# Kernel optimization log

Measured on AMD Instinct MI355X. Metric: run time of the kernel, lower is better.

The kernel has to match this reference:

```python
import jax, jax.numpy as jnp
import numpy as np

BATCH = 16
D_MODEL = 384
STATE = 64          # state_dim
D_INNER = 384       # ssd_expand * d_model
H = 64
W = 64


def setup_inputs() -> dict:
    key = jax.random.key(0)
    ks = jax.random.split(key, 6)
    x = jax.random.normal(ks[0], (BATCH, D_MODEL, H * W), jnp.float32)
    # 1x1 Conv1d weights stored as 2D matrices [out_ch, in_ch]
    W_bcdt = jax.random.normal(ks[1], (3 * STATE, D_MODEL), jnp.float32) / np.sqrt(D_MODEL).astype(np.float32)
    # depthwise 3x3 conv, groups = 3*STATE -> kernel [3S, 1, 3, 3]
    W_dw = jax.random.normal(ks[2], (3 * STATE, 1, 3, 3), jnp.float32) / 3.0
    W_hz = jax.random.normal(ks[3], (2 * D_INNER, D_MODEL), jnp.float32) / np.sqrt(D_MODEL).astype(np.float32)
    W_out = jax.random.normal(ks[4], (D_MODEL, D_INNER), jnp.float32) / np.sqrt(D_INNER).astype(np.float32)
    A_param = jax.random.uniform(ks[5], (STATE,), jnp.float32, 1.0, 16.0)
    D_param = jnp.ones((1,), jnp.float32)
    return {"x": x, "W_bcdt": W_bcdt, "W_dw": W_dw, "W_hz": W_hz,
            "W_out": W_out, "A_param": A_param, "D_param": D_param,
            "size_h": H, "size_w": W}


def reference(x, W_bcdt, W_dw, W_hz, W_out, A_param, D_param, size_h, size_w):
    b, d, L = x.shape
    S = A_param.shape[0]
    # BCdt_proj: 1x1 conv1d == matmul over channel dim -> [b, 3S, L]
    bcdt = jnp.einsum('od,bdl->bol', W_bcdt, x)
    # depthwise 3x3 conv over the spatial view [b, 3S, H, W]
    xhw = bcdt.reshape(b, 3 * S, size_h, size_w)
    xhw = jax.lax.conv_general_dilated(
        xhw, W_dw, window_strides=(1, 1), padding='SAME',
        dimension_numbers=('NCHW', 'OIHW', 'NCHW'),
        feature_group_count=3 * S)
    bcdt = xhw.reshape(b, 3 * S, L)
    Bm, Cm, dt = jnp.split(bcdt, 3, axis=1)          # each [b, S, L]
    # softmax over the sequence dim with learned A offset
    A = jax.nn.softmax(dt + A_param[None, :, None], axis=-1)
    AB = A * Bm                                       # [b, S, L]
    h = jnp.einsum('bdl,bsl->bds', x, AB)             # x @ AB^T -> [b, d, S]
    hz = jnp.einsum('od,bds->bos', W_hz, h)           # hz_proj -> [b, 2*d_inner, S]
    h1, z = jnp.split(hz, 2, axis=1)                  # each [b, d_inner, S]
    hgate = h1 * jax.nn.silu(z) + h1 * D_param[0]
    hout = jnp.einsum('oe,bes->bos', W_out, hgate)    # out_proj -> [b, d, S]
    y = jnp.einsum('bds,bsl->bdl', hout, Cm)          # h @ C -> [b, d, L]
    y = y.reshape(b, d, size_h, size_w)
    return (y, hout)
```

## Files before the change

kernel.cpp:

```cpp
#include <hip/hip_runtime.h>

typedef unsigned short u16;
typedef short s16x8 __attribute__((ext_vector_type(8)));
typedef float f32x4 __attribute__((ext_vector_type(4)));

#define NB 16
#define DMODEL 384
#define SDIM 64
#define LSEQ 4096
#define C3S 192

__device__ __forceinline__ float b2f(u16 u) {
    union { unsigned int i; float f; } v; v.i = ((unsigned int)u) << 16; return v.f;
}
__device__ __forceinline__ u16 f2b(float f) {
    union { float ff; unsigned int i; } v; v.ff = f;
    unsigned int x = v.i;
    unsigned int r = (x + 0x7fffu + ((x >> 16) & 1u)) >> 16;
    return (u16)r;
}

__global__ __launch_bounds__(256) void kcvt(const float* __restrict__ x,
                                            u16* __restrict__ xbT) {
    __shared__ __align__(16) u16 T[64][72];
    const int t = threadIdx.x;
    const int l0 = blockIdx.x * 64;
    const int d0 = blockIdx.y * 64;
    const int b = blockIdx.z;
    const int dr = t >> 2;
    const int lo = (t & 3) * 16;
    const float* xp = x + ((size_t)(b * DMODEL + d0 + dr)) * LSEQ + l0 + lo;
    float4 x0 = *reinterpret_cast<const float4*>(xp + 0);
    float4 x1 = *reinterpret_cast<const float4*>(xp + 4);
    float4 x2 = *reinterpret_cast<const float4*>(xp + 8);
    float4 x3 = *reinterpret_cast<const float4*>(xp + 12);
    s16x8 va, vb;
    va[0] = (short)f2b(x0.x); va[1] = (short)f2b(x0.y); va[2] = (short)f2b(x0.z); va[3] = (short)f2b(x0.w);
    va[4] = (short)f2b(x1.x); va[5] = (short)f2b(x1.y); va[6] = (short)f2b(x1.z); va[7] = (short)f2b(x1.w);
    vb[0] = (short)f2b(x2.x); vb[1] = (short)f2b(x2.y); vb[2] = (short)f2b(x2.z); vb[3] = (short)f2b(x2.w);
    vb[4] = (short)f2b(x3.x); vb[5] = (short)f2b(x3.y); vb[6] = (short)f2b(x3.z); vb[7] = (short)f2b(x3.w);
    *reinterpret_cast<s16x8*>(&T[dr][lo + 0]) = va;
    *reinterpret_cast<s16x8*>(&T[dr][lo + 8]) = vb;
    __syncthreads();
    const int lr = t >> 2;
    const int dof = (t & 3) * 16;
    s16x8 wa, wb;
    #pragma unroll
    for (int j = 0; j < 8; ++j) {
        wa[j] = (short)T[dof + j][lr];
        wb[j] = (short)T[dof + 8 + j][lr];
    }
    u16* xtp = xbT + ((size_t)(b * LSEQ + l0 + lr)) * DMODEL + d0 + dof;
    *reinterpret_cast<s16x8*>(xtp + 0) = wa;
    *reinterpret_cast<s16x8*>(xtp + 8) = wb;
}

__global__ __launch_bounds__(256) void k1_mfma(const u16* __restrict__ xbT,
                                               const float* __restrict__ Wb,
                                               u16* __restrict__ rawbc,
                                               float* __restrict__ rawdt) {
    __shared__ __align__(16) short As[64 * 40];
    __shared__ __align__(16) short Bs[256 * 40];
    const int t = threadIdx.x;
    const int l0 = blockIdx.x * 256;
    const int o0 = blockIdx.y * 64;
    const int b = blockIdx.z;
    const int lane = t & 63;
    const int w = t >> 6;
    const int wm = w >> 1, wn = w & 1;
    const int lm = lane & 15, kg = lane >> 4;
    f32x4 acc[2][8];
    #pragma unroll
    for (int i = 0; i < 2; ++i)
        #pragma unroll
        for (int j = 0; j < 8; ++j) acc[i][j] = (f32x4){0.f, 0.f, 0.f, 0.f};

    const int arow = t >> 2;
    const int aoff = (t & 3) * 8;
    const float* wp = Wb + (size_t)(o0 + arow) * DMODEL + aoff;
    const u16* bp = xbT + ((size_t)(b * LSEQ + l0)) * DMODEL;

    for (int kc = 0; kc < DMODEL; kc += 32) {
        float4 w0 = *reinterpret_cast<const float4*>(wp + kc);
        float4 w1 = *reinterpret_cast<const float4*>(wp + kc + 4);
        s16x8 av;
        av[0] = (short)f2b(w0.x); av[1] = (short)f2b(w0.y); av[2] = (short)f2b(w0.z); av[3] = (short)f2b(w0.w);
        av[4] = (short)f2b(w1.x); av[5] = (short)f2b(w1.y); av[6] = (short)f2b(w1.z); av[7] = (short)f2b(w1.w);
        *reinterpret_cast<s16x8*>(&As[arow * 40 + aoff]) = av;
        #pragma unroll
        for (int i = 0; i < 4; ++i) {
            int c = t + i * 256;
            int brow = c >> 2;
            int boff = (c & 3) * 8;
            s16x8 bv = *reinterpret_cast<const s16x8*>(bp + (size_t)brow * DMODEL + kc + boff);
            *reinterpret_cast<s16x8*>(&Bs[brow * 40 + boff]) = bv;
        }
        __syncthreads();
        s16x8 af[2], bf[8];
        #pragma unroll
        for (int i = 0; i < 2; ++i)
            af[i] = *reinterpret_cast<s16x8*>(&As[(wm * 32 + i * 16 + lm) * 40 + kg * 8]);
        #pragma unroll
        for (int j = 0; j < 8; ++j)
            bf[j] = *reinterpret_cast<s16x8*>(&Bs[(wn * 128 + j * 16 + lm) * 40 + kg * 8]);
        #pragma unroll
        for (int i = 0; i < 2; ++i)
            #pragma unroll
            for (int j = 0; j < 8; ++j)
                acc[i][j] = __builtin_amdgcn_mfma_f32_16x16x32_bf16(af[i], bf[j], acc[i][j], 0, 0, 0);
        __syncthreads();
    }
    #pragma unroll
    for (int i = 0; i < 2; ++i) {
        #pragma unroll
        for (int j = 0; j < 8; ++j) {
            #pragma unroll
            for (int r = 0; r < 4; ++r) {
                int o = o0 + wm * 32 + i * 16 + kg * 4 + r;
                int l = l0 + wn * 128 + j * 16 + lm;
                float val = acc[i][j][r];
                if (o < 128) rawbc[((size_t)b * 128 + o) * LSEQ + l] = f2b(val);
                else         rawdt[((size_t)b * 64 + (o - 128)) * LSEQ + l] = val;
            }
        }
    }
}

__global__ __launch_bounds__(256) void k2c_cm(const u16* __restrict__ rawbc,
                                              const float* __restrict__ Wdw,
                                              u16* __restrict__ CMB) {
    const int t = threadIdx.x;
    const int rg = blockIdx.x;
    const int c = blockIdx.y;
    const int b = blockIdx.z;
    const int row = rg * 4 + (t >> 6);
    const int col = t & 63;
    float w[9];
    #pragma unroll
    for (int k = 0; k < 9; ++k) w[k] = Wdw[(64 + c) * 9 + k];
    const u16* ip = rawbc + ((size_t)b * 128 + 64 + c) * LSEQ;
    float acc = 0.f;
    #pragma unroll
    for (int dy = -1; dy <= 1; ++dy) {
        int r = row + dy;
        if (r < 0 || r > 63) continue;
        #pragma unroll
        for (int dx = -1; dx <= 1; ++dx) {
            int cc = col + dx;
            if (cc < 0 || cc > 63) continue;
            acc = fmaf(w[(dy + 1) * 3 + (dx + 1)], b2f(ip[r * 64 + cc]), acc);
        }
    }
    CMB[((size_t)b * SDIM + c) * LSEQ + row * 64 + col] = f2b(acc);
}

__global__ __launch_bounds__(256) void kcmT(const u16* __restrict__ CMB,
                                            u16* __restrict__ CmT) {
    __shared__ __align__(16) u16 T[64][72];
    const int t = threadIdx.x;
    const int l0 = blockIdx.x * 64;
    const int b = blockIdx.y;
    const int sr = t >> 2;
    const int lo = (t & 3) * 16;
    const u16* ip = CMB + ((size_t)(b * SDIM + sr)) * LSEQ + l0 + lo;
    s16x8 va = *reinterpret_cast<const s16x8*>(ip);
    s16x8 vb = *reinterpret_cast<const s16x8*>(ip + 8);
    *reinterpret_cast<s16x8*>(&T[sr][lo + 0]) = va;
    *reinterpret_cast<s16x8*>(&T[sr][lo + 8]) = vb;
    __syncthreads();
    const int lr = t >> 2;
    const int sof = (t & 3) * 16;
    s16x8 wa, wb;
    #pragma unroll
    for (int j = 0; j < 8; ++j) {
        wa[j] = (short)T[sof + j][lr];
        wb[j] = (short)T[sof + 8 + j][lr];
    }
    u16* op = CmT + ((size_t)(b * LSEQ + l0 + lr)) * SDIM + sof;
    *reinterpret_cast<s16x8*>(op + 0) = wa;
    *reinterpret_cast<s16x8*>(op + 8) = wb;
}

__global__ __launch_bounds__(256) void k23_ab(const u16* __restrict__ rawbc,
                                              const float* __restrict__ rawdt,
                                              const float* __restrict__ Wdw,
                                              const float* __restrict__ Ap,
                                              u16* __restrict__ AB) {
    __shared__ float chB[LSEQ];
    __shared__ float chT[LSEQ];
    __shared__ float red[4];
    const int t = threadIdx.x;
    const int s = blockIdx.x;
    const int b = blockIdx.y;
    const u16* rB = rawbc + ((size_t)b * 128 + s) * LSEQ;
    const float* rT = rawdt + ((size_t)b * 64 + s) * LSEQ;
    #pragma unroll
    for (int i = 0; i < 16; ++i) {
        int idx = t + i * 256;
        chB[idx] = b2f(rB[idx]);
        chT[idx] = rT[idx];
    }
    __syncthreads();
    float wB[9], wT[9];
    #pragma unroll
    for (int k = 0; k < 9; ++k) {
        wB[k] = Wdw[s * 9 + k];
        wT[k] = Wdw[(128 + s) * 9 + k];
    }
    const float a = Ap[s];
    float vB[16], vT[16];
    float m = -3.0e38f;
    #pragma unroll
    for (int i = 0; i < 16; ++i) {
        int idx = t + i * 256;
        int row = idx >> 6, col = idx & 63;
        float aB = 0.f, aT = 0.f;
        #pragma unroll
        for (int dy = -1; dy <= 1; ++dy) {
            int r = row + dy;
            if (r < 0 || r > 63) continue;
            #pragma unroll
            for (int dx = -1; dx <= 1; ++dx) {
                int cc = col + dx;
                if (cc < 0 || cc > 63) continue;
                int p = r * 64 + cc;
                int wi = (dy + 1) * 3 + (dx + 1);
                aB = fmaf(wB[wi], chB[p], aB);
                aT = fmaf(wT[wi], chT[p], aT);
            }
        }
        vB[i] = aB;
        vT[i] = aT + a;
        m = fmaxf(m, vT[i]);
    }
    #pragma unroll
    for (int off = 32; off; off >>= 1) m = fmaxf(m, __shfl_xor(m, off));
    if ((t & 63) == 0) red[t >> 6] = m;
    __syncthreads();
    m = fmaxf(fmaxf(red[0], red[1]), fmaxf(red[2], red[3]));
    __syncthreads();
    float sum = 0.f;
    #pragma unroll
    for (int i = 0; i < 16; ++i) {
        vT[i] = expf(vT[i] - m);
        sum += vT[i];
    }
    #pragma unroll
    for (int off = 32; off; off >>= 1) sum += __shfl_xor(sum, off);
    if ((t & 63) == 0) red[t >> 6] = sum;
    __syncthreads();
    sum = red[0] + red[1] + red[2] + red[3];
    const float inv = 1.0f / sum;
    u16* op = AB + ((size_t)b * SDIM + s) * LSEQ;
    #pragma unroll
    for (int i = 0; i < 16; ++i) {
        int idx = t + i * 256;
        op[idx] = f2b(vT[i] * inv * vB[i]);
    }
}

__global__ __launch_bounds__(256) void k4_mfma(const float* __restrict__ x,
                                               const u16* __restrict__ ABu,
                                               float* __restrict__ hpart) {
    __shared__ __align__(16) short As[64 * 40];
    __shared__ __align__(16) short Bs[64 * 40];
    const int t = threadIdx.x;
    const int d0 = blockIdx.x * 64;
    const int kc = blockIdx.y;
    const int b = blockIdx.z;
    const int lane = t & 63;
    const int w = t >> 6;
    const int wm = w >> 1, wn = w & 1;
    const int lm = lane & 15, kg = lane >> 4;
    const int arow = t >> 2;
    const int aoff = (t & 3) * 8;
    const float* ap = x + ((size_t)(b * DMODEL + d0 + arow)) * LSEQ + kc * 1024 + aoff;
    const u16* bp = ABu + ((size_t)(b * SDIM + arow)) * LSEQ + kc * 1024 + aoff;
    f32x4 acc[2][2];
    #pragma unroll
    for (int i = 0; i < 2; ++i)
        #pragma unroll
        for (int j = 0; j < 2; ++j) acc[i][j] = (f32x4){0.f, 0.f, 0.f, 0.f};

    for (int ks = 0; ks < 1024; ks += 32) {
        float4 a0 = *reinterpret_cast<const float4*>(ap + ks);
        float4 a1 = *reinterpret_cast<const float4*>(ap + ks + 4);
        s16x8 av;
        av[0] = (short)f2b(a0.x); av[1] = (short)f2b(a0.y); av[2] = (short)f2b(a0.z); av[3] = (short)f2b(a0.w);
        av[4] = (short)f2b(a1.x); av[5] = (short)f2b(a1.y); av[6] = (short)f2b(a1.z); av[7] = (short)f2b(a1.w);
        s16x8 bv = *reinterpret_cast<const s16x8*>(bp + ks);
        *reinterpret_cast<s16x8*>(&As[arow * 40 + aoff]) = av;
        *reinterpret_cast<s16x8*>(&Bs[arow * 40 + aoff]) = bv;
        __syncthreads();
        s16x8 af[2], bf[2];
        #pragma unroll
        for (int i = 0; i < 2; ++i) {
            af[i] = *reinterpret_cast<s16x8*>(&As[(wm * 32 + i * 16 + lm) * 40 + kg * 8]);
            bf[i] = *reinterpret_cast<s16x8*>(&Bs[(wn * 32 + i * 16 + lm) * 40 + kg * 8]);
        }
        #pragma unroll
        for (int i = 0; i < 2; ++i)
            #pragma unroll
            for (int j = 0; j < 2; ++j)
                acc[i][j] = __builtin_amdgcn_mfma_f32_16x16x32_bf16(af[i], bf[j], acc[i][j], 0, 0, 0);
        __syncthreads();
    }
    #pragma unroll
    for (int i = 0; i < 2; ++i) {
        #pragma unroll
        for (int j = 0; j < 2; ++j) {
            int d = d0 + wm * 32 + i * 16 + kg * 4;
            int s = wn * 32 + j * 16 + lm;
            float* p = hpart + (size_t)kc * (1024 * DMODEL) + ((size_t)b * 64 + s) * DMODEL + d;
            *reinterpret_cast<f32x4*>(p) = acc[i][j];
        }
    }
}

__global__ __launch_bounds__(256) void k4r(const float* __restrict__ hp,
                                           u16* __restrict__ htb) {
    const int i = (blockIdx.x * 256 + threadIdx.x) * 4;
    const int N = 1024 * DMODEL;
    float4 v0 = *reinterpret_cast<const float4*>(hp + i);
    float4 v1 = *reinterpret_cast<const float4*>(hp + N + i);
    float4 v2 = *reinterpret_cast<const float4*>(hp + 2 * N + i);
    float4 v3 = *reinterpret_cast<const float4*>(hp + 3 * N + i);
    ushort4 o;
    o.x = f2b(v0.x + v1.x + v2.x + v3.x);
    o.y = f2b(v0.y + v1.y + v2.y + v3.y);
    o.z = f2b(v0.z + v1.z + v2.z + v3.z);
    o.w = f2b(v0.w + v1.w + v2.w + v3.w);
    *reinterpret_cast<ushort4*>(htb + i) = o;
}

__global__ __launch_bounds__(256) void k5hz(const u16* __restrict__ HTB,
                                            const float* __restrict__ Whz,
                                            float* __restrict__ HZT) {
    __shared__ __align__(16) short As[64 * 40];
    __shared__ __align__(16) short Bs[64 * 40];
    const int t = threadIdx.x;
    const int m0 = blockIdx.x * 64;
    const int n0 = blockIdx.y * 64;
    const int lane = t & 63;
    const int w = t >> 6;
    const int wm = w >> 1, wn = w & 1;
    const int lm = lane & 15, kg = lane >> 4;
    const int arow = t >> 2;
    const int aoff = (t & 3) * 8;
    const u16* apg = HTB + (size_t)(m0 + arow) * DMODEL + aoff;
    const float* bpg = Whz + (size_t)(n0 + arow) * DMODEL + aoff;
    f32x4 acc[2][2];
    #pragma unroll
    for (int i = 0; i < 2; ++i)
        #pragma unroll
        for (int j = 0; j < 2; ++j) acc[i][j] = (f32x4){0.f, 0.f, 0.f, 0.f};

    for (int kc = 0; kc < DMODEL; kc += 32) {
        s16x8 av = *reinterpret_cast<const s16x8*>(apg + kc);
        float4 b0 = *reinterpret_cast<const float4*>(bpg + kc);
        float4 b1 = *reinterpret_cast<const float4*>(bpg + kc + 4);
        s16x8 bv;
        bv[0] = (short)f2b(b0.x); bv[1] = (short)f2b(b0.y); bv[2] = (short)f2b(b0.z); bv[3] = (short)f2b(b0.w);
        bv[4] = (short)f2b(b1.x); bv[5] = (short)f2b(b1.y); bv[6] = (short)f2b(b1.z); bv[7] = (short)f2b(b1.w);
        *reinterpret_cast<s16x8*>(&As[arow * 40 + aoff]) = av;
        *reinterpret_cast<s16x8*>(&Bs[arow * 40 + aoff]) = bv;
        __syncthreads();
        s16x8 af[2], bf[2];
        #pragma unroll
        for (int i = 0; i < 2; ++i) {
            af[i] = *reinterpret_cast<s16x8*>(&As[(wm * 32 + i * 16 + lm) * 40 + kg * 8]);
            bf[i] = *reinterpret_cast<s16x8*>(&Bs[(wn * 32 + i * 16 + lm) * 40 + kg * 8]);
        }
        #pragma unroll
        for (int i = 0; i < 2; ++i)
            #pragma unroll
            for (int j = 0; j < 2; ++j)
                acc[i][j] = __builtin_amdgcn_mfma_f32_16x16x32_bf16(af[i], bf[j], acc[i][j], 0, 0, 0);
        __syncthreads();
    }
    #pragma unroll
    for (int i = 0; i < 2; ++i) {
        #pragma unroll
        for (int j = 0; j < 2; ++j) {
            #pragma unroll
            for (int r = 0; r < 4; ++r) {
                int bs = m0 + wm * 32 + i * 16 + kg * 4 + r;
                int o = n0 + wn * 32 + j * 16 + lm;
                HZT[(size_t)bs * 768 + o] = acc[i][j][r];
            }
        }
    }
}

__global__ __launch_bounds__(256) void k5g(const float* __restrict__ HZT,
                                           const float* __restrict__ Dp,
                                           u16* __restrict__ HGT) {
    const int i = (blockIdx.x * 256 + threadIdx.x) * 4;
    const int bs = i / DMODEL, d = i - bs * DMODEL;
    const float* p = HZT + (size_t)bs * 768 + d;
    float4 h1 = *reinterpret_cast<const float4*>(p);
    float4 z  = *reinterpret_cast<const float4*>(p + DMODEL);
    const float Dv = Dp[0];
    ushort4 o;
    o.x = f2b(h1.x * (z.x / (1.f + expf(-z.x)) + Dv));
    o.y = f2b(h1.y * (z.y / (1.f + expf(-z.y)) + Dv));
    o.z = f2b(h1.z * (z.z / (1.f + expf(-z.z)) + Dv));
    o.w = f2b(h1.w * (z.w / (1.f + expf(-z.w)) + Dv));
    *reinterpret_cast<ushort4*>(HGT + i) = o;
}

__global__ __launch_bounds__(256) void k5ho(const u16* __restrict__ HGT,
                                            const float* __restrict__ Wout,
                                            float* __restrict__ ho,
                                            u16* __restrict__ hob) {
    __shared__ __align__(16) short As[64 * 40];
    __shared__ __align__(16) short Bs[64 * 40];
    const int t = threadIdx.x;
    const int m0 = blockIdx.x * 64;
    const int n0 = blockIdx.y * 64;
    const int lane = t & 63;
    const int w = t >> 6;
    const int wm = w >> 1, wn = w & 1;
    const int lm = lane & 15, kg = lane >> 4;
    const int arow = t >> 2;
    const int aoff = (t & 3) * 8;
    const u16* apg = HGT + (size_t)(m0 + arow) * DMODEL + aoff;
    const float* bpg = Wout + (size_t)(n0 + arow) * DMODEL + aoff;
    f32x4 acc[2][2];
    #pragma unroll
    for (int i = 0; i < 2; ++i)
        #pragma unroll
        for (int j = 0; j < 2; ++j) acc[i][j] = (f32x4){0.f, 0.f, 0.f, 0.f};

    for (int kc = 0; kc < DMODEL; kc += 32) {
        s16x8 av = *reinterpret_cast<const s16x8*>(apg + kc);
        float4 b0 = *reinterpret_cast<const float4*>(bpg + kc);
        float4 b1 = *reinterpret_cast<const float4*>(bpg + kc + 4);
        s16x8 bv;
        bv[0] = (short)f2b(b0.x); bv[1] = (short)f2b(b0.y); bv[2] = (short)f2b(b0.z); bv[3] = (short)f2b(b0.w);
        bv[4] = (short)f2b(b1.x); bv[5] = (short)f2b(b1.y); bv[6] = (short)f2b(b1.z); bv[7] = (short)f2b(b1.w);
        *reinterpret_cast<s16x8*>(&As[arow * 40 + aoff]) = av;
        *reinterpret_cast<s16x8*>(&Bs[arow * 40 + aoff]) = bv;
        __syncthreads();
        s16x8 af[2], bf[2];
        #pragma unroll
        for (int i = 0; i < 2; ++i) {
            af[i] = *reinterpret_cast<s16x8*>(&As[(wm * 32 + i * 16 + lm) * 40 + kg * 8]);
            bf[i] = *reinterpret_cast<s16x8*>(&Bs[(wn * 32 + i * 16 + lm) * 40 + kg * 8]);
        }
        #pragma unroll
        for (int i = 0; i < 2; ++i)
            #pragma unroll
            for (int j = 0; j < 2; ++j)
                acc[i][j] = __builtin_amdgcn_mfma_f32_16x16x32_bf16(af[i], bf[j], acc[i][j], 0, 0, 0);
        __syncthreads();
    }
    #pragma unroll
    for (int i = 0; i < 2; ++i) {
        #pragma unroll
        for (int j = 0; j < 2; ++j) {
            int bs = m0 + wm * 32 + i * 16 + kg * 4;
            int b = bs >> 6, s = bs & 63;
            int o = n0 + wn * 32 + j * 16 + lm;
            size_t idx = ((size_t)b * DMODEL + o) * SDIM + s;
            *reinterpret_cast<f32x4*>(ho + idx) = acc[i][j];
            ushort4 u;
            u.x = f2b(acc[i][j][0]); u.y = f2b(acc[i][j][1]);
            u.z = f2b(acc[i][j][2]); u.w = f2b(acc[i][j][3]);
            *reinterpret_cast<ushort4*>(hob + idx) = u;
        }
    }
}

__global__ __launch_bounds__(256) void k6_mfma(const u16* __restrict__ CmT,
                                               const u16* __restrict__ hob,
                                               float* __restrict__ y) {
    const int t = threadIdx.x;
    const int l0 = blockIdx.x * 128;
    const int d0 = blockIdx.y * 128;
    const int b = blockIdx.z;
    const int lane = t & 63;
    const int w = t >> 6;
    const int wm = w >> 1, wn = w & 1;
    const int lm = lane & 15, kg = lane >> 4;
    const u16* hp = hob + (size_t)b * DMODEL * SDIM;
    const u16* cp = CmT + (size_t)b * LSEQ * SDIM;
    s16x8 af[4][2], bf[4][2];
    #pragma unroll
    for (int i = 0; i < 4; ++i)
        #pragma unroll
        for (int ks = 0; ks < 2; ++ks)
            af[i][ks] = *reinterpret_cast<const s16x8*>(
                hp + (size_t)(d0 + wm * 64 + i * 16 + lm) * SDIM + ks * 32 + kg * 8);
    #pragma unroll
    for (int j = 0; j < 4; ++j)
        #pragma unroll
        for (int ks = 0; ks < 2; ++ks)
            bf[j][ks] = *reinterpret_cast<const s16x8*>(
                cp + (size_t)(l0 + wn * 64 + j * 16 + lm) * SDIM + ks * 32 + kg * 8);
    f32x4 acc[4][4];
    #pragma unroll
    for (int i = 0; i < 4; ++i)
        #pragma unroll
        for (int j = 0; j < 4; ++j) acc[i][j] = (f32x4){0.f, 0.f, 0.f, 0.f};
    #pragma unroll
    for (int ks = 0; ks < 2; ++ks)
        #pragma unroll
        for (int i = 0; i < 4; ++i)
            #pragma unroll
            for (int j = 0; j < 4; ++j)
                acc[i][j] = __builtin_amdgcn_mfma_f32_16x16x32_bf16(af[i][ks], bf[j][ks], acc[i][j], 0, 0, 0);
    float* yp = y + (size_t)b * DMODEL * LSEQ;
    #pragma unroll
    for (int i = 0; i < 4; ++i) {
        #pragma unroll
        for (int j = 0; j < 4; ++j) {
            #pragma unroll
            for (int r = 0; r < 4; ++r) {
                int d = d0 + wm * 64 + i * 16 + kg * 4 + r;
                int l = l0 + wn * 64 + j * 16 + lm;
                yp[(size_t)d * LSEQ + l] = acc[i][j][r];
            }
        }
    }
}

extern "C" void kernel_launch(void* const* d_in, const int* in_sizes, int n_in,
                              void* d_out, int out_size, void* d_ws, size_t ws_size,
                              hipStream_t stream) {
    const float* x    = (const float*)d_in[0];
    const float* Wb   = (const float*)d_in[1];
    const float* Wdw  = (const float*)d_in[2];
    const float* Whz  = (const float*)d_in[3];
    const float* Wout = (const float*)d_in[4];
    const float* Ap   = (const float*)d_in[5];
    const float* Dp   = (const float*)d_in[6];

    float* out = (float*)d_out;
    const size_t YSIZE = (size_t)NB * DMODEL * LSEQ;

    u16*   RAWBC  = (u16*)out;
    float* RAWDT  = out + 4194304;
    u16*   XBT    = (u16*)(out + 8388608);
    u16*   CMB    = (u16*)(out + 8388608);
    u16*   ABu    = (u16*)(out + 20971520);
    float* HPART  = out;
    u16*   HTB    = (u16*)(out + 1572864);
    float* HZT    = out + 1769472;
    u16*   HGT    = (u16*)(out + 2555904);
    float* HO     = out + YSIZE;
    u16*   CmT    = (u16*)d_ws;
    u16*   HOB    = (u16*)d_ws + 4194304;

    kcvt   <<<dim3(64, 6, NB), 256, 0, stream>>>(x, XBT);
    k1_mfma<<<dim3(16, 3, NB), 256, 0, stream>>>(XBT, Wb, RAWBC, RAWDT);
    k2c_cm <<<dim3(16, SDIM, NB), 256, 0, stream>>>(RAWBC, Wdw, CMB);
    kcmT   <<<dim3(64, NB), 256, 0, stream>>>(CMB, CmT);
    k23_ab <<<dim3(SDIM, NB), 256, 0, stream>>>(RAWBC, RAWDT, Wdw, Ap, ABu);
    k4_mfma<<<dim3(6, 4, NB), 256, 0, stream>>>(x, ABu, HPART);
    k4r    <<<dim3(384), 256, 0, stream>>>(HPART, HTB);
    k5hz   <<<dim3(16, 12), 256, 0, stream>>>(HTB, Whz, HZT);
    k5g    <<<dim3(384), 256, 0, stream>>>(HZT, Dp, HGT);
    k5ho   <<<dim3(16, 6), 256, 0, stream>>>(HGT, Wout, HO, HOB);
    k6_mfma<<<dim3(32, 3, NB), 256, 0, stream>>>(CmT, HOB, out);
}
```

Measured before the change: 171.3 us.

## Compute all BCdt channels per k1 block and split k4 reduction eight ways

k1 now runs 512-thread blocks that each compute all 192 output channels for a 256-position tile. The x tile is loaded once instead of three times across channel blocks, at the cost of fewer blocks (256) and more accumulators per thread. k4 splits the sequence reduction into 8 chunks of 512 instead of 4 of 1024, raising block count for better occupancy. The partial-sum reducer now sums 8 partials, and the scratch offsets move to fit the larger partial buffer.

```diff
diff --git a/kernel.cpp b/kernel.cpp
--- a/kernel.cpp
+++ b/kernel.cpp
@@ -55,68 +55,71 @@
     *reinterpret_cast<s16x8*>(xtp + 8) = wb;
 }
 
-__global__ __launch_bounds__(256) void k1_mfma(const u16* __restrict__ xbT,
+__global__ __launch_bounds__(512) void k1_mfma(const u16* __restrict__ xbT,
                                                const float* __restrict__ Wb,
                                                u16* __restrict__ rawbc,
                                                float* __restrict__ rawdt) {
-    __shared__ __align__(16) short As[64 * 40];
+    __shared__ __align__(16) short As[192 * 40];
     __shared__ __align__(16) short Bs[256 * 40];
     const int t = threadIdx.x;
     const int l0 = blockIdx.x * 256;
-    const int o0 = blockIdx.y * 64;
-    const int b = blockIdx.z;
+    const int b = blockIdx.y;
     const int lane = t & 63;
     const int w = t >> 6;
     const int wm = w >> 1, wn = w & 1;
     const int lm = lane & 15, kg = lane >> 4;
-    f32x4 acc[2][8];
-    #pragma unroll
-    for (int i = 0; i < 2; ++i)
+    f32x4 acc[3][8];
+    #pragma unroll
+    for (int i = 0; i < 3; ++i)
         #pragma unroll
         for (int j = 0; j < 8; ++j) acc[i][j] = (f32x4){0.f, 0.f, 0.f, 0.f};
 
-    const int arow = t >> 2;
-    const int aoff = (t & 3) * 8;
-    const float* wp = Wb + (size_t)(o0 + arow) * DMODEL + aoff;
     const u16* bp = xbT + ((size_t)(b * LSEQ + l0)) * DMODEL;
+    const int brow = t >> 1;
+    const int boff = (t & 1) * 16;
 
     for (int kc = 0; kc < DMODEL; kc += 32) {
-        float4 w0 = *reinterpret_cast<const float4*>(wp + kc);
-        float4 w1 = *reinterpret_cast<const float4*>(wp + kc + 4);
-        s16x8 av;
-        av[0] = (short)f2b(w0.x); av[1] = (short)f2b(w0.y); av[2] = (short)f2b(w0.z); av[3] = (short)f2b(w0.w);
-        av[4] = (short)f2b(w1.x); av[5] = (short)f2b(w1.y); av[6] = (short)f2b(w1.z); av[7] = (short)f2b(w1.w);
-        *reinterpret_cast<s16x8*>(&As[arow * 40 + aoff]) = av;
-        #pragma unroll
-        for (int i = 0; i < 4; ++i) {
-            int c = t + i * 256;
-            int brow = c >> 2;
-            int boff = (c & 3) * 8;
-            s16x8 bv = *reinterpret_cast<const s16x8*>(bp + (size_t)brow * DMODEL + kc + boff);
-            *reinterpret_cast<s16x8*>(&Bs[brow * 40 + boff]) = bv;
-        }
-        __syncthreads();
-        s16x8 af[2], bf[8];
-        #pragma unroll
-        for (int i = 0; i < 2; ++i)
-            af[i] = *reinterpret_cast<s16x8*>(&As[(wm * 32 + i * 16 + lm) * 40 + kg * 8]);
+        if (t < 192) {
+            const float* wp = Wb + (size_t)t * DMODEL + kc;
+            #pragma unroll
+            for (int c = 0; c < 4; ++c) {
+                float4 w0 = *reinterpret_cast<const float4*>(wp + c * 8);
+                float4 w1 = *reinterpret_cast<const float4*>(wp + c * 8 + 4);
+                s16x8 av;
+                av[0] = (short)f2b(w0.x); av[1] = (short)f2b(w0.y); av[2] = (short)f2b(w0.z); av[3] = (short)f2b(w0.w);
+                av[4] = (short)f2b(w1.x); av[5] = (short)f2b(w1.y); av[6] = (short)f2b(w1.z); av[7] = (short)f2b(w1.w);
+                *reinterpret_cast<s16x8*>(&As[t * 40 + c * 8]) = av;
+            }
+        }
+        {
+            const u16* src = bp + (size_t)brow * DMODEL + kc + boff;
+            s16x8 bv0 = *reinterpret_cast<const s16x8*>(src);
+            s16x8 bv1 = *reinterpret_cast<const s16x8*>(src + 8);
+            *reinterpret_cast<s16x8*>(&Bs[brow * 40 + boff]) = bv0;
+            *reinterpret_cast<s16x8*>(&Bs[brow * 40 + boff + 8]) = bv1;
+        }
+        __syncthreads();
+        s16x8 af[3], bf[8];
+        #pragma unroll
+        for (int i = 0; i < 3; ++i)
+            af[i] = *reinterpret_cast<s16x8*>(&As[(wm * 48 + i * 16 + lm) * 40 + kg * 8]);
         #pragma unroll
         for (int j = 0; j < 8; ++j)
             bf[j] = *reinterpret_cast<s16x8*>(&Bs[(wn * 128 + j * 16 + lm) * 40 + kg * 8]);
         #pragma unroll
-        for (int i = 0; i < 2; ++i)
+        for (int i = 0; i < 3; ++i)
             #pragma unroll
             for (int j = 0; j < 8; ++j)
                 acc[i][j] = __builtin_amdgcn_mfma_f32_16x16x32_bf16(af[i], bf[j], acc[i][j], 0, 0, 0);
         __syncthreads();
     }
     #pragma unroll
-    for (int i = 0; i < 2; ++i) {
+    for (int i = 0; i < 3; ++i) {
         #pragma unroll
         for (int j = 0; j < 8; ++j) {
             #pragma unroll
             for (int r = 0; r < 4; ++r) {
-                int o = o0 + wm * 32 + i * 16 + kg * 4 + r;
+                int o = wm * 48 + i * 16 + kg * 4 + r;
                 int l = l0 + wn * 128 + j * 16 + lm;
                 float val = acc[i][j][r];
                 if (o < 128) rawbc[((size_t)b * 128 + o) * LSEQ + l] = f2b(val);
@@ -274,15 +277,15 @@
     const int lm = lane & 15, kg = lane >> 4;
     const int arow = t >> 2;
     const int aoff = (t & 3) * 8;
-    const float* ap = x + ((size_t)(b * DMODEL + d0 + arow)) * LSEQ + kc * 1024 + aoff;
-    const u16* bp = ABu + ((size_t)(b * SDIM + arow)) * LSEQ + kc * 1024 + aoff;
+    const float* ap = x + ((size_t)(b * DMODEL + d0 + arow)) * LSEQ + kc * 512 + aoff;
+    const u16* bp = ABu + ((size_t)(b * SDIM + arow)) * LSEQ + kc * 512 + aoff;
     f32x4 acc[2][2];
     #pragma unroll
     for (int i = 0; i < 2; ++i)
         #pragma unroll
         for (int j = 0; j < 2; ++j) acc[i][j] = (f32x4){0.f, 0.f, 0.f, 0.f};
 
-    for (int ks = 0; ks < 1024; ks += 32) {
+    for (int ks = 0; ks < 512; ks += 32) {
         float4 a0 = *reinterpret_cast<const float4*>(ap + ks);
         float4 a1 = *reinterpret_cast<const float4*>(ap + ks + 4);
         s16x8 av;
@@ -321,15 +324,14 @@
                                            u16* __restrict__ htb) {
     const int i = (blockIdx.x * 256 + threadIdx.x) * 4;
     const int N = 1024 * DMODEL;
-    float4 v0 = *reinterpret_cast<const float4*>(hp + i);
-    float4 v1 = *reinterpret_cast<const float4*>(hp + N + i);
-    float4 v2 = *reinterpret_cast<const float4*>(hp + 2 * N + i);
-    float4 v3 = *reinterpret_cast<const float4*>(hp + 3 * N + i);
+    float sx = 0.f, sy = 0.f, sz = 0.f, sw = 0.f;
+    #pragma unroll
+    for (int kc = 0; kc < 8; ++kc) {
+        float4 v = *reinterpret_cast<const float4*>(hp + (size_t)kc * N + i);
+        sx += v.x; sy += v.y; sz += v.z; sw += v.w;
+    }
     ushort4 o;
-    o.x = f2b(v0.x + v1.x + v2.x + v3.x);
-    o.y = f2b(v0.y + v1.y + v2.y + v3.y);
-    o.z = f2b(v0.z + v1.z + v2.z + v3.z);
-    o.w = f2b(v0.w + v1.w + v2.w + v3.w);
+    o.x = f2b(sx); o.y = f2b(sy); o.z = f2b(sz); o.w = f2b(sw);
     *reinterpret_cast<ushort4*>(htb + i) = o;
 }
 
@@ -545,19 +547,19 @@
     u16*   CMB    = (u16*)(out + 8388608);
     u16*   ABu    = (u16*)(out + 20971520);
     float* HPART  = out;
-    u16*   HTB    = (u16*)(out + 1572864);
-    float* HZT    = out + 1769472;
-    u16*   HGT    = (u16*)(out + 2555904);
+    u16*   HTB    = (u16*)(out + 3145728);
+    float* HZT    = out + 3342336;
+    u16*   HGT    = (u16*)(out + 4128768);
     float* HO     = out + YSIZE;
     u16*   CmT    = (u16*)d_ws;
     u16*   HOB    = (u16*)d_ws + 4194304;
 
     kcvt   <<<dim3(64, 6, NB), 256, 0, stream>>>(x, XBT);
-    k1_mfma<<<dim3(16, 3, NB), 256, 0, stream>>>(XBT, Wb, RAWBC, RAWDT);
+    k1_mfma<<<dim3(16, NB), 512, 0, stream>>>(XBT, Wb, RAWBC, RAWDT);
     k2c_cm <<<dim3(16, SDIM, NB), 256, 0, stream>>>(RAWBC, Wdw, CMB);
     kcmT   <<<dim3(64, NB), 256, 0, stream>>>(CMB, CmT);
     k23_ab <<<dim3(SDIM, NB), 256, 0, stream>>>(RAWBC, RAWDT, Wdw, Ap, ABu);
-    k4_mfma<<<dim3(6, 4, NB), 256, 0, stream>>>(x, ABu, HPART);
+    k4_mfma<<<dim3(6, 8, NB), 256, 0, stream>>>(x, ABu, HPART);
     k4r    <<<dim3(384), 256, 0, stream>>>(HPART, HTB);
     k5hz   <<<dim3(16, 12), 256, 0, stream>>>(HTB, Whz, HZT);
     k5g    <<<dim3(384), 256, 0, stream>>>(HZT, Dp, HGT);
```

Result: slower. 176.1 us (+2.8%).
